# Performance work log

Measured on AMD Instinct MI355X. Metric: run time of the kernel, lower is better.

The kernel has to match this reference:

```python
import jax, jax.numpy as jnp
import numpy as np

DIM_MODEL = 1024
NUM_HEADS = 16
DIM_HEAD = 64
B, S = 2, 2048


def setup_inputs() -> dict:
    key = jax.random.key(0)
    ks = jax.random.split(key, 10)
    scale = 1.0 / np.sqrt(DIM_MODEL)
    inp = {
        "x": jax.random.normal(ks[0], (B, S, DIM_MODEL), dtype=jnp.float32),
        "padding_mask": jax.random.randint(ks[1], (B, S), 0, 2, dtype=jnp.int32),
        "Wq": jax.random.normal(ks[2], (DIM_MODEL, DIM_MODEL), dtype=jnp.float32) * scale,
        "bq": jnp.zeros((DIM_MODEL,), dtype=jnp.float32),
        "Wk": jax.random.normal(ks[3], (DIM_MODEL, DIM_MODEL), dtype=jnp.float32) * scale,
        "bk": jnp.zeros((DIM_MODEL,), dtype=jnp.float32),
        "Wv": jax.random.normal(ks[4], (DIM_MODEL, DIM_MODEL), dtype=jnp.float32) * scale,
        "bv": jnp.zeros((DIM_MODEL,), dtype=jnp.float32),
        "Wo": jax.random.normal(ks[5], (DIM_MODEL, DIM_MODEL), dtype=jnp.float32) * scale,
        "bo": jnp.zeros((DIM_MODEL,), dtype=jnp.float32),
    }
    return inp


def reference(x, padding_mask, Wq, bq, Wk, bk, Wv, bv, Wo, bo):
    b, s, _ = x.shape
    dot_scale = jnp.sqrt(jnp.asarray(DIM_HEAD, dtype=x.dtype))
    # projections -> (b, h, s, d)
    q = (x @ Wq + bq).reshape(b, s, NUM_HEADS, DIM_HEAD).transpose(0, 2, 1, 3)
    k = (x @ Wk + bk).reshape(b, s, NUM_HEADS, DIM_HEAD).transpose(0, 2, 1, 3)
    v = (x @ Wv + bv).reshape(b, s, NUM_HEADS, DIM_HEAD).transpose(0, 2, 1, 3)
    # scores (b, h, s, s)
    scores = jnp.einsum("bhqd,bhkd->bhqk", q, k) / dot_scale
    mask = (padding_mask == 1)[:, None, None, :]  # (b,1,1,s) over key positions
    scores = jnp.where(mask, -jnp.inf, scores)
    attn = jax.nn.softmax(scores, axis=-1)
    out = jnp.einsum("bhqk,bhkd->bhqd", attn, v)
    out = out.transpose(0, 2, 1, 3).reshape(b, s, NUM_HEADS * DIM_HEAD)
    return out @ Wo + bo
```

## Files before the change

kernel.cpp:

```cpp
#include <hip/hip_runtime.h>
#include <hip/hip_bf16.h>
#include <stdint.h>
#include <math.h>

#define D_MODEL 1024
#define NHEAD   16
#define DHEAD   64
#define BATCH   2
#define SEQ     2048
#define M_TOK   (BATCH * SEQ)

#define QSCALE 0.18033688011112042f

typedef __attribute__((ext_vector_type(8))) short   short8;
typedef __attribute__((ext_vector_type(8))) __bf16  bf16x8;
typedef __attribute__((ext_vector_type(4))) float   f32x4;

__device__ inline short f2bf(float f) {
  unsigned int u = __builtin_bit_cast(unsigned int, f);
  unsigned int r = (u + 0x7FFFu + ((u >> 16) & 1u)) >> 16;
  return (short)(unsigned short)r;
}
__device__ inline short f2bf_fast(float f) {
  unsigned int u = __builtin_bit_cast(unsigned int, f);
  return (short)(unsigned short)((u + 0x8000u) >> 16);
}

__device__ inline void gl_lds16(const void* g, void* l) {
  __builtin_amdgcn_global_load_lds((__attribute__((address_space(1))) void*)(g),
                                   (__attribute__((address_space(3))) void*)(l),
                                   16, 0, 0);
}

__device__ inline bf16x8 lds_frag(const short* p) {
  return *(const bf16x8*)(p);
}

__global__ __launch_bounds__(256) void prep(const float* __restrict__ x,
                                            short* __restrict__ xb,
                                            const float* __restrict__ w0,
                                            const float* __restrict__ w1,
                                            const float* __restrict__ w2,
                                            const float* __restrict__ w3,
                                            short* __restrict__ out) {
  const int t = threadIdx.x;
  if (blockIdx.z == 4) {
    size_t base = ((size_t)blockIdx.y * 16 + blockIdx.x) * 16384;
    const float* in = x + base;
    short* o = xb + base;
#pragma unroll
    for (int i = 0; i < 16; ++i) {
      f32x4 v = *(const f32x4*)(in + (size_t)t * 4 + i * 1024);
      short4 s4;
      s4.x = f2bf(v[0]); s4.y = f2bf(v[1]); s4.z = f2bf(v[2]); s4.w = f2bf(v[3]);
      *(short4*)(o + (size_t)t * 4 + i * 1024) = s4;
    }
    return;
  }
  __shared__ short tile[64][72];
  const float* W = blockIdx.z == 0 ? w0 : blockIdx.z == 1 ? w1 : blockIdx.z == 2 ? w2 : w3;
  short* O = out + (size_t)blockIdx.z * (D_MODEL * (size_t)D_MODEL);
  int n0 = blockIdx.x * 64, k0 = blockIdx.y * 64;
#pragma unroll
  for (int i = 0; i < 16; ++i) {
    int idx = t + 256 * i;
    int r = idx >> 6, c = idx & 63;
    tile[r][c] = f2bf(W[(size_t)(k0 + r) * D_MODEL + n0 + c]);
  }
  __syncthreads();
#pragma unroll
  for (int i = 0; i < 16; ++i) {
    int idx = t + 256 * i;
    int r = idx >> 6, c = idx & 63;
    O[(size_t)(n0 + r) * D_MODEL + k0 + c] = tile[c][r];
  }
}

template <bool OUTF32, bool VT, int TN>
__global__ __launch_bounds__(256) void gemm128(const short* __restrict__ A,
                                               const short* __restrict__ Bt_base,
                                               const float* __restrict__ b0,
                                               const float* __restrict__ b1,
                                               const float* __restrict__ b2,
                                               void* __restrict__ out_base,
                                               short* __restrict__ vt,
                                               const int* __restrict__ pm) {
  constexpr int NI = TN / 32;
  const int z = blockIdx.z;
  const short* Bt   = Bt_base + (size_t)z * (D_MODEL * (size_t)D_MODEL);
  const float* bias = (z == 0) ? b0 : (z == 1) ? b1 : b2;

  __shared__ short As[128 * 64];
  __shared__ short Bs[TN * 64];

  const int t = threadIdx.x;
  const int lane = t & 63;
  const int wid = t >> 6;
  const int wm = (wid >> 1) * 64, wn = (wid & 1) * (TN / 2);
  const int m0 = blockIdx.x * 128, n0 = blockIdx.y * TN;
  const int cl = lane & 15, q = lane >> 4;
  const int sw = cl & 7;

  f32x4 acc[4][NI];
#pragma unroll
  for (int i = 0; i < 4; ++i)
#pragma unroll
    for (int j = 0; j < NI; ++j) acc[i][j] = 0.0f;

  for (int k0 = 0; k0 < D_MODEL; k0 += 64) {
    __syncthreads();
#pragma unroll
    for (int i = 0; i < 4; ++i) {
      int c = t + 256 * i;
      int row = c >> 3, cp = c & 7;
      int col = ((cp ^ (row & 7)) * 8);
      gl_lds16(A + (size_t)(m0 + row) * D_MODEL + k0 + col, (void*)(As + c * 8));
    }
#pragma unroll
    for (int i = 0; i < NI; ++i) {
      int c = t + 256 * i;
      int row = c >> 3, cp = c & 7;
      int col = ((cp ^ (row & 7)) * 8);
      gl_lds16(Bt + (size_t)(n0 + row) * D_MODEL + k0 + col, (void*)(Bs + c * 8));
    }
    __syncthreads();

    bf16x8 af[4][2], bfr[NI][2];
#pragma unroll
    for (int mi = 0; mi < 4; ++mi) {
      af[mi][0] = lds_frag(As + (wm + mi * 16 + cl) * 64 + (q ^ sw) * 8);
      af[mi][1] = lds_frag(As + (wm + mi * 16 + cl) * 64 + ((4 + q) ^ sw) * 8);
    }
#pragma unroll
    for (int ni = 0; ni < NI; ++ni) {
      bfr[ni][0] = lds_frag(Bs + (wn + ni * 16 + cl) * 64 + (q ^ sw) * 8);
      bfr[ni][1] = lds_frag(Bs + (wn + ni * 16 + cl) * 64 + ((4 + q) ^ sw) * 8);
    }
#pragma unroll
    for (int mi = 0; mi < 4; ++mi)
#pragma unroll
      for (int ni = 0; ni < NI; ++ni) {
        acc[mi][ni] = __builtin_amdgcn_mfma_f32_16x16x32_bf16(af[mi][0], bfr[ni][0], acc[mi][ni], 0, 0, 0);
        acc[mi][ni] = __builtin_amdgcn_mfma_f32_16x16x32_bf16(af[mi][1], bfr[ni][1], acc[mi][ni], 0, 0, 0);
      }
  }

  const float oscale = (VT && z == 0) ? QSCALE : 1.0f;
  int4 mm[4];
  if (VT && z == 2) {
#pragma unroll
    for (int mi = 0; mi < 4; ++mi) {
      int rbase = m0 + wm + mi * 16 + q * 4;
      mm[mi] = *(const int4*)(pm + (size_t)(rbase >> 11) * SEQ + (rbase & (SEQ - 1)));
    }
  }
#pragma unroll
  for (int ni = 0; ni < NI; ++ni) {
    int col = n0 + wn + ni * 16 + cl;
    float bv = bias[col];
#pragma unroll
    for (int mi = 0; mi < 4; ++mi) {
      int rbase = m0 + wm + mi * 16 + q * 4;
      if (VT && z == 2) {
        short4 o4;
        o4.x = (mm[mi].x == 1) ? (short)0 : f2bf_fast(acc[mi][ni][0] + bv);
        o4.y = (mm[mi].y == 1) ? (short)0 : f2bf_fast(acc[mi][ni][1] + bv);
        o4.z = (mm[mi].z == 1) ? (short)0 : f2bf_fast(acc[mi][ni][2] + bv);
        o4.w = (mm[mi].w == 1) ? (short)0 : f2bf_fast(acc[mi][ni][3] + bv);
        int btok = rbase >> 11;
        int s    = rbase & (SEQ - 1);
        int sp = (s & ~31) | ((s & 16) >> 2) | ((s & 12) << 1) | (s & 3);
        *(short4*)(vt + (size_t)btok * ((size_t)D_MODEL * SEQ) + (size_t)col * SEQ + sp) = o4;
      } else {
#pragma unroll
        for (int r = 0; r < 4; ++r) {
          float v = (acc[mi][ni][r] + bv) * oscale;
          size_t idx = (size_t)(rbase + r) * D_MODEL + col;
          if (OUTF32) {
            ((float*)out_base)[idx] = v;
          } else {
            short* out = (short*)out_base + (size_t)z * ((size_t)M_TOK * D_MODEL);
            out[idx] = f2bf_fast(v);
          }
        }
      }
    }
  }
}

__global__ __launch_bounds__(512) void attn_flash(const short* __restrict__ Q,
                                                  const short* __restrict__ K,
                                                  const short* __restrict__ Vt,
                                                  const int*   __restrict__ mask,
                                                  short* __restrict__ ctx) {
  const int qb = blockIdx.x;
  const int h  = blockIdx.y;
  const int b  = blockIdx.z;

  __shared__ __align__(16) short smem[36864];
  short* bufA = smem;
  short* bufB = smem + 16384;
  float* Usf  = (float*)(smem + 32768);

  const int t = threadIdx.x;
  const int lane = t & 63;
  const int wid = t >> 6;
  const int wg  = wid >> 1;
  const int kvh = wid & 1;
  const int cl = lane & 15, q = lane >> 4;
  const int sw = cl & 7;

  const size_t rowQ0 = (size_t)b * SEQ + (size_t)qb * 128;
  const size_t rowK0 = (size_t)b * SEQ;
  const size_t vbase = ((size_t)b * D_MODEL + h * DHEAD) * SEQ;

  const int srow = t >> 3, scp = t & 7;
  const int scol = (scp ^ (srow & 7)) * 8;
  const short* Kg0 = K + (rowK0 + srow) * D_MODEL + h * DHEAD + scol;
  const short* Kg1 = K + (rowK0 + 1024 + srow) * D_MODEL + h * DHEAD + scol;
  const short* Vg0 = Vt + vbase + (size_t)srow * SEQ + scol;
  const short* Vg1 = Vt + vbase + (size_t)srow * SEQ + 1024 + scol;

  auto stage = [&](short* buf, int sn) {
    gl_lds16(Kg0 + (size_t)sn * D_MODEL, (void*)(buf + t * 8));
    gl_lds16(Kg1 + (size_t)sn * D_MODEL, (void*)(buf + 4096 + t * 8));
    gl_lds16(Vg0 + sn,                   (void*)(buf + 8192 + t * 8));
    gl_lds16(Vg1 + sn,                   (void*)(buf + 8192 + 4096 + t * 8));
  };

  stage(bufA, 0);
#pragma unroll
  for (int i = 0; i < 2; ++i) {
    int c = t + 512 * i;
    int row = c >> 3, cp = c & 7;
    gl_lds16(Q + (rowQ0 + row) * D_MODEL + h * DHEAD + ((cp ^ (row & 7)) * 8),
             (void*)(bufB + c * 8));
  }
  {
    int4 mv = *(const int4*)(mask + (size_t)b * SEQ + t * 4);
    f32x4 u4;
    u4[0] = (mv.x == 1) ? -1e30f : 0.0f;
    u4[1] = (mv.y == 1) ? -1e30f : 0.0f;
    u4[2] = (mv.z == 1) ? -1e30f : 0.0f;
    u4[3] = (mv.w == 1) ? -1e30f : 0.0f;
    *(f32x4*)(Usf + t * 4) = u4;
  }
  __syncthreads();

  bf16x8 qf[2][2];
#pragma unroll
  for (int rb = 0; rb < 2; ++rb) {
    int row = wg * 32 + rb * 16 + cl;
    qf[rb][0] = lds_frag(bufB + row * 64 + (q ^ sw) * 8);
    qf[rb][1] = lds_frag(bufB + row * 64 + ((4 + q) ^ sw) * 8);
  }

  f32x4 lacc[2], oacc[2][4];
#pragma unroll
  for (int rb = 0; rb < 2; ++rb) {
    lacc[rb] = 0.0f;
#pragma unroll
    for (int dj = 0; dj < 4; ++dj) oacc[rb][dj] = 0.0f;
  }

  auto compute = [&](const short* buf, int s0) {
    const short* Kp = buf + kvh * 4096;
    const short* Vp = buf + 8192 + kvh * 4096;
    const float* Bp = Usf + kvh * 1024 + s0 + 4 * q;

    f32x4 s[2][4];
#pragma unroll
    for (int j = 0; j < 4; ++j) {
      bf16x8 kf0 = lds_frag(Kp + (j * 16 + cl) * 64 + (q ^ sw) * 8);
      bf16x8 kf1 = lds_frag(Kp + (j * 16 + cl) * 64 + ((4 + q) ^ sw) * 8);
      f32x4 cv = *(const f32x4*)(Bp + j * 16);
#pragma unroll
      for (int rb = 0; rb < 2; ++rb) {
        f32x4 sa = cv;
        sa = __builtin_amdgcn_mfma_f32_16x16x32_bf16(kf0, qf[rb][0], sa, 0, 0, 0);
        sa = __builtin_amdgcn_mfma_f32_16x16x32_bf16(kf1, qf[rb][1], sa, 0, 0, 0);
        s[rb][j] = sa;
      }
    }

#pragma unroll
    for (int rb = 0; rb < 2; ++rb)
#pragma unroll
      for (int j = 0; j < 4; ++j) {
#pragma unroll
        for (int r = 0; r < 4; ++r)
          s[rb][j][r] = __builtin_amdgcn_exp2f(s[rb][j][r]);
        lacc[rb] += s[rb][j];
      }

    bf16x8 pf[2][2];
#pragma unroll
    for (int rb = 0; rb < 2; ++rb)
#pragma unroll
      for (int c = 0; c < 2; ++c) {
        bf16x8 v;
        v[0] = (__bf16)s[rb][2 * c][0];
        v[1] = (__bf16)s[rb][2 * c][1];
        v[2] = (__bf16)s[rb][2 * c][2];
        v[3] = (__bf16)s[rb][2 * c][3];
        v[4] = (__bf16)s[rb][2 * c + 1][0];
        v[5] = (__bf16)s[rb][2 * c + 1][1];
        v[6] = (__bf16)s[rb][2 * c + 1][2];
        v[7] = (__bf16)s[rb][2 * c + 1][3];
        pf[rb][c] = v;
      }

#pragma unroll
    for (int dj = 0; dj < 4; ++dj) {
      const short* vrow = Vp + (dj * 16 + cl) * 64;
#pragma unroll
      for (int c = 0; c < 2; ++c) {
        bf16x8 vfc = lds_frag(vrow + (((4 * c + q) ^ sw) * 8));
#pragma unroll
        for (int rb = 0; rb < 2; ++rb)
          oacc[rb][dj] = __builtin_amdgcn_mfma_f32_16x16x32_bf16(vfc, pf[rb][c], oacc[rb][dj], 0, 0, 0);
      }
    }
  };

  for (int it = 0; it < 8; ++it) {
    int s0 = it * 128;
    __syncthreads();
    stage(bufB, s0 + 64);
    compute(bufA, s0);
    __syncthreads();
    if (it < 7) stage(bufA, s0 + 128);
    compute(bufB, s0 + 64);
  }

  __syncthreads();
  float hl[2];
#pragma unroll
  for (int rb = 0; rb < 2; ++rb)
    hl[rb] = lacc[rb][0] + lacc[rb][1] + lacc[rb][2] + lacc[rb][3];

  float* redO = (float*)smem;
  float* redL = (float*)(smem + 16384);
  const int slot = wg * 64 + lane;
  if (kvh) {
#pragma unroll
    for (int rb = 0; rb < 2; ++rb) {
#pragma unroll
      for (int dj = 0; dj < 4; ++dj) {
        int qi = (rb * 4 + dj) ^ (lane & 7);
        *(f32x4*)(redO + slot * 32 + qi * 4) = oacc[rb][dj];
      }
      redL[slot * 2 + rb] = hl[rb];
    }
  }
  __syncthreads();
  if (kvh) return;
#pragma unroll
  for (int rb = 0; rb < 2; ++rb) {
    hl[rb] += redL[slot * 2 + rb];
#pragma unroll
    for (int dj = 0; dj < 4; ++dj) {
      int qi = (rb * 4 + dj) ^ (lane & 7);
      oacc[rb][dj] += *(const f32x4*)(redO + slot * 32 + qi * 4);
    }
  }
#pragma unroll
  for (int rb = 0; rb < 2; ++rb) {
    hl[rb] += __shfl_xor(hl[rb], 16);
    hl[rb] += __shfl_xor(hl[rb], 32);
  }

#pragma unroll
  for (int rb = 0; rb < 2; ++rb) {
    float inv = (hl[rb] > 0.0f) ? 1.0f / hl[rb] : 0.0f;
    size_t row = rowQ0 + wg * 32 + rb * 16 + cl;
#pragma unroll
    for (int dj = 0; dj < 4; ++dj) {
      short4 o4;
      o4.x = f2bf(oacc[rb][dj][0] * inv);
      o4.y = f2bf(oacc[rb][dj][1] * inv);
      o4.z = f2bf(oacc[rb][dj][2] * inv);
      o4.w = f2bf(oacc[rb][dj][3] * inv);
      *(short4*)(ctx + row * D_MODEL + h * DHEAD + dj * 16 + q * 4) = o4;
    }
  }
}

extern "C" void kernel_launch(void* const* d_in, const int* in_sizes, int n_in,
                              void* d_out, int out_size, void* d_ws, size_t ws_size,
                              hipStream_t stream) {
  (void)in_sizes; (void)n_in; (void)out_size; (void)ws_size;

  const float* x  = (const float*)d_in[0];
  const int*   pm = (const int*)  d_in[1];
  const float* Wq = (const float*)d_in[2];
  const float* bq = (const float*)d_in[3];
  const float* Wk = (const float*)d_in[4];
  const float* bk = (const float*)d_in[5];
  const float* Wv = (const float*)d_in[6];
  const float* bv = (const float*)d_in[7];
  const float* Wo = (const float*)d_in[8];
  const float* bo = (const float*)d_in[9];

  const size_t WMAT = (size_t)D_MODEL * D_MODEL;
  const size_t TOKD = (size_t)M_TOK * D_MODEL;

  short* base = (short*)d_ws;
  short* Wt = base;
  short* xb = base + 4 * WMAT;
  short* Qw = xb + TOKD;
  short* Kw = Qw + TOKD;
  short* Vtw = Kw + TOKD;
  short* Cw = Vtw + TOKD;

  prep<<<dim3(16, 16, 5), 256, 0, stream>>>(x, xb, Wq, Wk, Wv, Wo, Wt);
  gemm128<false, true, 128><<<dim3(M_TOK / 128, D_MODEL / 128, 3), 256, 0, stream>>>(
      xb, Wt, bq, bk, bv, Qw, Vtw, pm);
  attn_flash<<<dim3(SEQ / 128, NHEAD, BATCH), 512, 0, stream>>>(Qw, Kw, Vtw, pm, Cw);
  gemm128<true, false, 64><<<dim3(M_TOK / 128, D_MODEL / 64, 1), 256, 0, stream>>>(
      Cw, Wt + 3 * WMAT, bo, bo, bo, d_out, nullptr, nullptr);
}
```

Measured before the change: 192.7 us.

## Double-buffer GEMM LDS tiles with K=32 stages to overlap loads and MFMA

The bf16 projection GEMM main loop now uses two shared-memory buffers with 32-wide K slices, so the next slice's global-to-LDS loads are issued before the current slice's MFMAs run. This drops one of the two barriers per step and hides load latency behind compute. The shared-memory layout is re-swizzled to pack row pairs into 64-element lines, which changes the LDS fragment addressing. In exchange there are twice as many loop iterations, each with half the MFMA work, and correctness now relies on the barrier also waiting for the asynchronous LDS loads.

```diff
diff --git a/kernel.cpp b/kernel.cpp
--- a/kernel.cpp
+++ b/kernel.cpp
@@ -85,13 +85,14 @@
                                                void* __restrict__ out_base,
                                                short* __restrict__ vt,
                                                const int* __restrict__ pm) {
-  constexpr int NI = TN / 32;
+  constexpr int NI  = TN / 32;
+  constexpr int NBI = (TN * 4) / 256;
   const int z = blockIdx.z;
   const short* Bt   = Bt_base + (size_t)z * (D_MODEL * (size_t)D_MODEL);
   const float* bias = (z == 0) ? b0 : (z == 1) ? b1 : b2;
 
-  __shared__ short As[128 * 64];
-  __shared__ short Bs[TN * 64];
+  __shared__ short As[2][128 * 32];
+  __shared__ short Bs[2][TN * 32];
 
   const int t = threadIdx.x;
   const int lane = t & 63;
@@ -99,7 +100,6 @@
   const int wm = (wid >> 1) * 64, wn = (wid & 1) * (TN / 2);
   const int m0 = blockIdx.x * 128, n0 = blockIdx.y * TN;
   const int cl = lane & 15, q = lane >> 4;
-  const int sw = cl & 7;
 
   f32x4 acc[4][NI];
 #pragma unroll
@@ -107,42 +107,52 @@
 #pragma unroll
     for (int j = 0; j < NI; ++j) acc[i][j] = 0.0f;
 
-  for (int k0 = 0; k0 < D_MODEL; k0 += 64) {
+  auto stage = [&](int ks) {
+    const int bi = ks & 1;
+    const int k0 = ks * 32;
+#pragma unroll
+    for (int i = 0; i < 2; ++i) {
+      int d = t + 256 * i;
+      int rp = d >> 3, x = (d & 7) ^ (rp & 7);
+      gl_lds16(A + (size_t)(m0 + rp * 2 + (x >> 2)) * D_MODEL + k0 + (x & 3) * 8,
+               (void*)(As[bi] + d * 8));
+    }
+#pragma unroll
+    for (int i = 0; i < NBI; ++i) {
+      int d = t + 256 * i;
+      int rp = d >> 3, x = (d & 7) ^ (rp & 7);
+      gl_lds16(Bt + (size_t)(n0 + rp * 2 + (x >> 2)) * D_MODEL + k0 + (x & 3) * 8,
+               (void*)(Bs[bi] + d * 8));
+    }
+  };
+
+  stage(0);
+  for (int ks = 0; ks < 32; ++ks) {
     __syncthreads();
-#pragma unroll
-    for (int i = 0; i < 4; ++i) {
-      int c = t + 256 * i;
-      int row = c >> 3, cp = c & 7;
-      int col = ((cp ^ (row & 7)) * 8);
-      gl_lds16(A + (size_t)(m0 + row) * D_MODEL + k0 + col, (void*)(As + c * 8));
-    }
-#pragma unroll
-    for (int i = 0; i < NI; ++i) {
-      int c = t + 256 * i;
-      int row = c >> 3, cp = c & 7;
-      int col = ((cp ^ (row & 7)) * 8);
-      gl_lds16(Bt + (size_t)(n0 + row) * D_MODEL + k0 + col, (void*)(Bs + c * 8));
-    }
-    __syncthreads();
-
-    bf16x8 af[4][2], bfr[NI][2];
+    if (ks + 1 < 32) stage(ks + 1);
+    const short* Ap = As[ks & 1];
+    const short* Bp = Bs[ks & 1];
+
+    bf16x8 af[4], bfr[NI];
 #pragma unroll
     for (int mi = 0; mi < 4; ++mi) {
-      af[mi][0] = lds_frag(As + (wm + mi * 16 + cl) * 64 + (q ^ sw) * 8);
-      af[mi][1] = lds_frag(As + (wm + mi * 16 + cl) * 64 + ((4 + q) ^ sw) * 8);
+      int row = wm + mi * 16 + cl;
+      int rp = row >> 1;
+      int pos = (((row & 1) << 2) | q) ^ (rp & 7);
+      af[mi] = lds_frag(Ap + rp * 64 + pos * 8);
     }
 #pragma unroll
     for (int ni = 0; ni < NI; ++ni) {
-      bfr[ni][0] = lds_frag(Bs + (wn + ni * 16 + cl) * 64 + (q ^ sw) * 8);
-      bfr[ni][1] = lds_frag(Bs + (wn + ni * 16 + cl) * 64 + ((4 + q) ^ sw) * 8);
+      int row = wn + ni * 16 + cl;
+      int rp = row >> 1;
+      int pos = (((row & 1) << 2) | q) ^ (rp & 7);
+      bfr[ni] = lds_frag(Bp + rp * 64 + pos * 8);
     }
 #pragma unroll
     for (int mi = 0; mi < 4; ++mi)
 #pragma unroll
-      for (int ni = 0; ni < NI; ++ni) {
-        acc[mi][ni] = __builtin_amdgcn_mfma_f32_16x16x32_bf16(af[mi][0], bfr[ni][0], acc[mi][ni], 0, 0, 0);
-        acc[mi][ni] = __builtin_amdgcn_mfma_f32_16x16x32_bf16(af[mi][1], bfr[ni][1], acc[mi][ni], 0, 0, 0);
-      }
+      for (int ni = 0; ni < NI; ++ni)
+        acc[mi][ni] = __builtin_amdgcn_mfma_f32_16x16x32_bf16(af[mi], bfr[ni], acc[mi][ni], 0, 0, 0);
   }
 
   const float oscale = (VT && z == 0) ? QSCALE : 1.0f;
```

After: 197.6 us. +2.5%, slower.
